# Optimization experiments

Hardware: AMD Instinct MI355X
Metric: run time of the kernel (lower is better)

## Reference

```python
import jax, jax.numpy as jnp
import numpy as np

B = 16384
SIZES = [512, 256, 256, 128]  # layer_sizes, layer 0 = clamped input
K = 16        # settling iterations
ETA = 0.1     # eta_x, scale 'none' => effective eta per layer = 0.1
CLIP = 1.0    # dx_clip


def setup_inputs() -> dict:
    key = jax.random.key(0)
    k0, k1, k2, k3 = jax.random.split(key, 4)
    x0 = jax.random.normal(k0, (B, SIZES[0]), jnp.float32)
    # W[l]: (D_{l+1}, D_l), init scale 1/sqrt(D_{l+1}) as in torch code
    W0 = jax.random.normal(k1, (SIZES[1], SIZES[0]), jnp.float32) * (1.0 / np.sqrt(SIZES[1]))
    W1 = jax.random.normal(k2, (SIZES[2], SIZES[1]), jnp.float32) * (1.0 / np.sqrt(SIZES[2]))
    W2 = jax.random.normal(k3, (SIZES[3], SIZES[2]), jnp.float32) * (1.0 / np.sqrt(SIZES[3]))
    return {"x0": x0, "W0": W0, "W1": W1, "W2": W2}


def _f(z):
    return jnp.tanh(z)


def _f_prime(z):
    t = jnp.tanh(z)
    return 1.0 - t * t


def _settle(x0, Ws):
    """Run K settling steps. Layer 0 clamped to x0; layers 1..L free."""
    L = len(Ws)
    bsz = x0.shape[0]
    xs0 = (x0,) + tuple(jnp.zeros((bsz, w.shape[0]), x0.dtype) for w in Ws)

    def step(xs, _):
        xs = list(xs)
        # top-down predictions: preact[l] = x[l+1] @ W[l], shape (B, D_l)
        preacts = [xs[l + 1] @ Ws[l] for l in range(L)]
        errs = [xs[l] - _f(preacts[l]) for l in range(L)]
        new = [xs[0]]  # layer 0 clamped
        for l in range(1, L + 1):
            # feedback: (e[l-1] * f'(preact[l-1])) @ W[l-1].T  (tied weights)
            dx = (errs[l - 1] * _f_prime(preacts[l - 1])) @ Ws[l - 1].T
            if l < L:
                dx = dx - errs[l]
            dx = jnp.clip(dx, -CLIP, CLIP)
            new.append(xs[l] + ETA * dx)
        return tuple(new), None

    final, _ = jax.lax.scan(step, xs0, None, length=K)
    return final


def reference(x0, W0, W1, W2):
    final = _settle(x0, (W0, W1, W2))
    # return settled latent (layer L) state, shape (B, 128)
    return final[-1]
```

## Files before the change

kernel.cpp:

```cpp
#include <hip/hip_runtime.h>

typedef _Float16 half8 __attribute__((ext_vector_type(8)));
typedef float floatx4 __attribute__((ext_vector_type(4)));

#define DEV_INLINE __device__ __forceinline__

constexpr int D0 = 512, D1 = 256, D2 = 256, D3 = 128;
constexpr int NROWS = 16384;
constexpr int MBLK = 32;
constexpr int NBLK = NROWS / MBLK;
constexpr int KITERS = 16;
constexpr float ETA = 0.1f;

constexpr int OFF_WF0 = 0;
constexpr int OFF_WF1 = OFF_WF0 + D1 * D0;
constexpr int OFF_WF2 = OFF_WF1 + D2 * D1;
constexpr int OFF_WB0 = OFF_WF2 + D3 * D2;
constexpr int OFF_WB1 = OFF_WB0 + D0 * D1;
constexpr int OFF_WB2 = OFF_WB1 + D1 * D2;
constexpr int PACK_ELEMS = OFF_WB2 + D2 * D3;

__global__ void repack_kernel(const float* __restrict__ W0, const float* __restrict__ W1,
                              const float* __restrict__ W2, _Float16* __restrict__ pack) {
  int p = blockIdx.x * 256 + threadIdx.x;
  if (p >= PACK_ELEMS) return;
  const float* W; int Csrc, Nd, off; bool tr;
  if (p < OFF_WF1)      { W = W0; Csrc = D0; Nd = D0; off = OFF_WF0; tr = false; }
  else if (p < OFF_WF2) { W = W1; Csrc = D1; Nd = D1; off = OFF_WF1; tr = false; }
  else if (p < OFF_WB0) { W = W2; Csrc = D2; Nd = D2; off = OFF_WF2; tr = false; }
  else if (p < OFF_WB1) { W = W0; Csrc = D0; Nd = D1; off = OFF_WB0; tr = true;  }
  else if (p < OFF_WB2) { W = W1; Csrc = D1; Nd = D1; off = OFF_WB1; tr = true;  }
  else                  { W = W2; Csrc = D2; Nd = D3; off = OFF_WB2; tr = true;  }
  int local = p - off;
  int j  = local & 7;
  int l  = (local >> 3) & 63;
  int fr = local >> 9;
  int NT = Nd >> 4;
  int nt = fr % NT, kt = fr / NT;
  int k = kt * 32 + ((l >> 4) << 3) + j;
  int n = nt * 16 + (l & 15);
  float v = tr ? W[n * Csrc + k] : W[k * Csrc + n];
  pack[p] = (_Float16)v;
}

DEV_INLINE float fast_tanh(float x) {
  float e = __expf(2.f * x);
  return 1.f - 2.f * __builtin_amdgcn_rcpf(e + 1.f);
}

DEV_INLINE void gl_lds16(const _Float16* g, char* l) {
  __builtin_amdgcn_global_load_lds(
      (const __attribute__((address_space(1))) unsigned int*)g,
      (__attribute__((address_space(3))) unsigned int*)l, 16, 0, 0);
}

template <int RT, int KSTEPS, int NTT, int STRB, int ASd>
DEV_INLINE void mm_staged(const char* __restrict__ A, const _Float16* __restrict__ Bp,
                          int nt, int lane, char* __restrict__ wslot, floatx4* acc) {
  const int arow = lane & 15;
  const int aoff = (lane >> 4) << 4;
  const _Float16* bsrc = Bp + ((size_t)nt * 64 + lane) * 8;
  gl_lds16(bsrc, wslot);
#pragma unroll
  for (int k0 = 0; k0 < KSTEPS; ++k0) {
    if (k0 + 1 < KSTEPS) {
      gl_lds16(bsrc + (size_t)(k0 + 1) * NTT * 512, wslot + ((k0 + 1) & 1) * 1024);
      asm volatile("s_waitcnt vmcnt(1)" ::: "memory");
    } else {
      asm volatile("s_waitcnt vmcnt(0)" ::: "memory");
    }
    __builtin_amdgcn_sched_barrier(0);
    const half8 b = *(const half8*)(wslot + (k0 & 1) * 1024 + lane * 16);
#pragma unroll
    for (int rt = 0; rt < RT; ++rt) {
      int row = rt * 16 + arow;
      int byte = (row * STRB + k0 * 64 + aoff) ^ ((row & 7) << 4);
      half8 a = *(const half8*)(A + byte);
      acc[rt * ASd] = __builtin_amdgcn_mfma_f32_16x16x32_f16(a, b, acc[rt * ASd], 0, 0, 0);
    }
    asm volatile("" ::: "memory");
    __builtin_amdgcn_sched_barrier(0);
  }
}

__global__ __launch_bounds__(512)
void settle_kernel(const float* __restrict__ x0,
                   const _Float16* __restrict__ pack,
                   float* __restrict__ out) {
  extern __shared__ char lds[];
  char* AX1 = lds;
  char* AG0 = lds + 16384;
  char* AQ  = lds + 24576;
  char* AG1 = lds + 40960;
  char* AR  = lds + 57344;
  char* WSL = lds + 65536;

  const int tid  = threadIdx.x;
  const int lane = tid & 63;
  const int wave = tid >> 6;
  const int row0 = blockIdx.x * MBLK;
  const int rsub = (lane >> 4) << 2;
  const int csub = lane & 15;
  char* ws = WSL + wave * 2048;

  half8 x0r[4];
#pragma unroll
  for (int q = 0; q < 4; ++q)
#pragma unroll
    for (int rt = 0; rt < 2; ++rt)
#pragma unroll
      for (int i = 0; i < 4; ++i) {
        int row = rt * 16 + rsub + i;
        int col = (q * 8 + wave) * 16 + csub;
        float v = x0[(size_t)(row0 + row) * D0 + col];
        int li = (q * 2 + rt) * 4 + i;
        x0r[li >> 3][li & 7] = (_Float16)v;
      }

  {
    floatx4 z = {0.f, 0.f, 0.f, 0.f};
    for (int i = tid; i < 1024; i += 512) ((floatx4*)AQ)[i] = z;
    for (int i = tid; i < 512; i += 512) ((floatx4*)AR)[i] = z;
  }

  const floatx4 zf = {0.f, 0.f, 0.f, 0.f};
  floatx4 x3m[2];
#pragma unroll
  for (int i = 0; i < 2; ++i) x3m[i] = zf;

  const _Float16* Wf0 = pack + OFF_WF0;
  const _Float16* Wf1 = pack + OFF_WF1;
  const _Float16* Wf2 = pack + OFF_WF2;
  const _Float16* Wb0 = pack + OFF_WB0;
  const _Float16* Wb1 = pack + OFF_WB1;
  const _Float16* Wb2 = pack + OFF_WB2;

  {
    floatx4 dx1a[4];
#pragma unroll
    for (int i = 0; i < 4; ++i) dx1a[i] = zf;
    for (int q = 0; q < 4; ++q) {
#pragma unroll
      for (int rt = 0; rt < 2; ++rt)
#pragma unroll
        for (int i = 0; i < 4; ++i) {
          int row = rt * 16 + rsub + i;
          int colq = wave * 16 + csub;
          int li = (q * 2 + rt) * 4 + i;
          int byte = (row * 256 + colq * 2) ^ ((row & 7) << 4);
          *(_Float16*)(AG0 + byte) = x0r[li >> 3][li & 7];
        }
      __syncthreads();
#pragma unroll
      for (int ct = 0; ct < 2; ++ct)
        mm_staged<2, 4, 16, 256, 2>(AG0, Wb0 + q * 32768, wave * 2 + ct, lane, ws, &dx1a[ct]);
      __syncthreads();
    }
#pragma unroll
    for (int rt = 0; rt < 2; ++rt)
#pragma unroll
      for (int ct = 0; ct < 2; ++ct) {
        int col = (wave * 2 + ct) * 16 + csub;
#pragma unroll
        for (int i = 0; i < 4; ++i) {
          int row = rt * 16 + rsub + i;
          float dx = fminf(1.f, fmaxf(-1.f, dx1a[rt * 2 + ct][i]));
          int byte = (row * 512 + col * 2) ^ ((row & 7) << 4);
          *(_Float16*)(AX1 + byte) = (_Float16)(ETA * dx);
        }
      }
    __syncthreads();
  }

  for (int it = 1; it < KITERS; ++it) {
    floatx4 dx1a[4];
    {
#pragma unroll
      for (int i = 0; i < 4; ++i) dx1a[i] = zf;
#pragma unroll
      for (int ct = 0; ct < 2; ++ct)
        mm_staged<2, 8, 16, 512, 2>(AQ, Wf1, wave * 2 + ct, lane, ws, &dx1a[ct]);
#pragma unroll
      for (int rt = 0; rt < 2; ++rt)
#pragma unroll
        for (int ct = 0; ct < 2; ++ct) {
          int col = (wave * 2 + ct) * 16 + csub;
#pragma unroll
          for (int i = 0; i < 4; ++i) {
            int row = rt * 16 + rsub + i;
            int sb = (row * 512 + col * 2) ^ ((row & 7) << 4);
            float t = fast_tanh(dx1a[rt * 2 + ct][i]);
            float x1o = (float)*(const _Float16*)(AX1 + sb);
            float e = x1o - t;
            *(_Float16*)(AG1 + sb) = (_Float16)(e * (1.f - t * t));
            dx1a[rt * 2 + ct][i] = -e;
          }
        }
    }
    for (int q = 0; q < 4; ++q) {
      {
        floatx4 acc3[2];
#pragma unroll
        for (int i = 0; i < 2; ++i) acc3[i] = zf;
        mm_staged<2, 8, 32, 512, 1>(AX1, Wf0, q * 8 + wave, lane, ws, acc3);
        int colq = wave * 16 + csub;
#pragma unroll
        for (int rt = 0; rt < 2; ++rt)
#pragma unroll
          for (int i = 0; i < 4; ++i) {
            int row = rt * 16 + rsub + i;
            int li = (q * 2 + rt) * 4 + i;
            float t = fast_tanh(acc3[rt][i]);
            float xv = (float)x0r[li >> 3][li & 7];
            float g = (xv - t) * (1.f - t * t);
            int byte = (row * 256 + colq * 2) ^ ((row & 7) << 4);
            *(_Float16*)(AG0 + byte) = (_Float16)g;
          }
      }
      __syncthreads();
#pragma unroll
      for (int ct = 0; ct < 2; ++ct)
        mm_staged<2, 4, 16, 256, 2>(AG0, Wb0 + q * 32768, wave * 2 + ct, lane, ws, &dx1a[ct]);
      __syncthreads();
    }
#pragma unroll
    for (int rt = 0; rt < 2; ++rt)
#pragma unroll
      for (int ct = 0; ct < 2; ++ct) {
        int col = (wave * 2 + ct) * 16 + csub;
#pragma unroll
        for (int i = 0; i < 4; ++i) {
          int row = rt * 16 + rsub + i;
          int sb = (row * 512 + col * 2) ^ ((row & 7) << 4);
          float dx = fminf(1.f, fmaxf(-1.f, dx1a[rt * 2 + ct][i]));
          float x1o = (float)*(const _Float16*)(AX1 + sb);
          *(_Float16*)(AX1 + sb) = (_Float16)(x1o + ETA * dx);
        }
      }
    floatx4 dx2a[4];
    half8 g2h[2];
    {
      floatx4 p2[4];
#pragma unroll
      for (int i = 0; i < 4; ++i) p2[i] = zf;
#pragma unroll
      for (int ct = 0; ct < 2; ++ct)
        mm_staged<2, 4, 16, 256, 2>(AR, Wf2, wave * 2 + ct, lane, ws, &p2[ct]);
#pragma unroll
      for (int rt = 0; rt < 2; ++rt)
#pragma unroll
        for (int ct = 0; ct < 2; ++ct) {
          int col = (wave * 2 + ct) * 16 + csub;
#pragma unroll
          for (int i = 0; i < 4; ++i) {
            int row = rt * 16 + rsub + i;
            int sb = (row * 512 + col * 2) ^ ((row & 7) << 4);
            float t = fast_tanh(p2[rt * 2 + ct][i]);
            float x2o = (float)*(const _Float16*)(AQ + sb);
            float e = x2o - t;
            int li = (rt * 2 + ct) * 4 + i;
            g2h[li >> 3][li & 7] = (_Float16)(e * (1.f - t * t));
            dx2a[rt * 2 + ct][i] = -e;
          }
        }
    }
    {
#pragma unroll
      for (int ct = 0; ct < 2; ++ct)
        mm_staged<2, 8, 16, 512, 2>(AG1, Wb1, wave * 2 + ct, lane, ws, &dx2a[ct]);
#pragma unroll
      for (int rt = 0; rt < 2; ++rt)
#pragma unroll
        for (int ct = 0; ct < 2; ++ct) {
          int col = (wave * 2 + ct) * 16 + csub;
#pragma unroll
          for (int i = 0; i < 4; ++i) {
            int row = rt * 16 + rsub + i;
            int sb = (row * 512 + col * 2) ^ ((row & 7) << 4);
            float dx = fminf(1.f, fmaxf(-1.f, dx2a[rt * 2 + ct][i]));
            float x2o = (float)*(const _Float16*)(AQ + sb);
            *(_Float16*)(AQ + sb) = (_Float16)(x2o + ETA * dx);
          }
        }
    }
    __syncthreads();
#pragma unroll
    for (int rt = 0; rt < 2; ++rt)
#pragma unroll
      for (int ct = 0; ct < 2; ++ct) {
        int col = (wave * 2 + ct) * 16 + csub;
#pragma unroll
        for (int i = 0; i < 4; ++i) {
          int row = rt * 16 + rsub + i;
          int sb = (row * 512 + col * 2) ^ ((row & 7) << 4);
          int li = (rt * 2 + ct) * 4 + i;
          *(_Float16*)(AG1 + sb) = g2h[li >> 3][li & 7];
        }
      }
    __syncthreads();
    {
      floatx4 acc6[2];
#pragma unroll
      for (int i = 0; i < 2; ++i) acc6[i] = zf;
      mm_staged<2, 8, 8, 512, 1>(AG1, Wb2, wave, lane, ws, acc6);
      __syncthreads();
      int col = wave * 16 + csub;
#pragma unroll
      for (int rt = 0; rt < 2; ++rt)
#pragma unroll
        for (int i = 0; i < 4; ++i) {
          int row = rt * 16 + rsub + i;
          float dx = fminf(1.f, fmaxf(-1.f, acc6[rt][i]));
          float nv = x3m[rt][i] + ETA * dx;
          x3m[rt][i] = nv;
          int byte = (row * 256 + col * 2) ^ ((row & 7) << 4);
          *(_Float16*)(AR + byte) = (_Float16)nv;
        }
    }
  }

  {
    int col = wave * 16 + csub;
#pragma unroll
    for (int rt = 0; rt < 2; ++rt)
#pragma unroll
      for (int i = 0; i < 4; ++i) {
        int row = rt * 16 + rsub + i;
        out[(size_t)(row0 + row) * D3 + col] = x3m[rt][i];
      }
  }
}

extern "C" void kernel_launch(void* const* d_in, const int* in_sizes, int n_in,
                              void* d_out, int out_size, void* d_ws, size_t ws_size,
                              hipStream_t stream) {
  const float* x0 = (const float*)d_in[0];
  const float* W0 = (const float*)d_in[1];
  const float* W1 = (const float*)d_in[2];
  const float* W2 = (const float*)d_in[3];
  float* out = (float*)d_out;

  _Float16* pack = (_Float16*)d_ws;
  repack_kernel<<<(PACK_ELEMS + 255) / 256, 256, 0, stream>>>(W0, W1, W2, pack);

  (void)hipFuncSetAttribute(reinterpret_cast<const void*>(settle_kernel),
                            hipFuncAttributeMaxDynamicSharedMemorySize, 81920);
  settle_kernel<<<NBLK, 512, 81920, stream>>>(x0, pack, out);
}
```

Before: 1.098 ms.

## Load weight fragments directly into registers instead of LDS double-buffering

Replaces the per-wave global_load_lds double-buffered staging of weight fragments with plain vector loads of all K-step B fragments into registers up front, followed by the MFMA loop. This removes the explicit vmcnt waits and sched barriers so the compiler can schedule loads freely. LDS use per block drops from 80KB to 64KB, which may allow more blocks per CU. In exchange it raises register pressure (up to 8 half8 B fragments held live) and exposes global/L2 latency at the start of each matmul.

```diff
diff --git a/kernel.cpp b/kernel.cpp
--- a/kernel.cpp
+++ b/kernel.cpp
@@ -48,38 +48,32 @@
   return 1.f - 2.f * __builtin_amdgcn_rcpf(e + 1.f);
 }
 
-DEV_INLINE void gl_lds16(const _Float16* g, char* l) {
-  __builtin_amdgcn_global_load_lds(
-      (const __attribute__((address_space(1))) unsigned int*)g,
-      (__attribute__((address_space(3))) unsigned int*)l, 16, 0, 0);
+DEV_INLINE const _Float16* bpt(const _Float16* Bp, int nt, int lane) {
+  return Bp + ((size_t)nt * 64 + lane) * 8;
 }
 
 template <int RT, int KSTEPS, int NTT, int STRB, int ASd>
-DEV_INLINE void mm_staged(const char* __restrict__ A, const _Float16* __restrict__ Bp,
-                          int nt, int lane, char* __restrict__ wslot, floatx4* acc) {
+DEV_INLINE void mm_reg(const char* __restrict__ A, const _Float16* __restrict__ bsrc,
+                       int lane, floatx4* acc) {
   const int arow = lane & 15;
   const int aoff = (lane >> 4) << 4;
-  const _Float16* bsrc = Bp + ((size_t)nt * 64 + lane) * 8;
-  gl_lds16(bsrc, wslot);
+  half8 bq[KSTEPS];
+#pragma unroll
+  for (int s = 0; s < KSTEPS; ++s)
+    bq[s] = *(const half8*)(bsrc + (size_t)s * NTT * 512);
 #pragma unroll
   for (int k0 = 0; k0 < KSTEPS; ++k0) {
-    if (k0 + 1 < KSTEPS) {
-      gl_lds16(bsrc + (size_t)(k0 + 1) * NTT * 512, wslot + ((k0 + 1) & 1) * 1024);
-      asm volatile("s_waitcnt vmcnt(1)" ::: "memory");
-    } else {
-      asm volatile("s_waitcnt vmcnt(0)" ::: "memory");
-    }
-    __builtin_amdgcn_sched_barrier(0);
-    const half8 b = *(const half8*)(wslot + (k0 & 1) * 1024 + lane * 16);
+    half8 a[RT];
 #pragma unroll
     for (int rt = 0; rt < RT; ++rt) {
       int row = rt * 16 + arow;
       int byte = (row * STRB + k0 * 64 + aoff) ^ ((row & 7) << 4);
-      half8 a = *(const half8*)(A + byte);
-      acc[rt * ASd] = __builtin_amdgcn_mfma_f32_16x16x32_f16(a, b, acc[rt * ASd], 0, 0, 0);
-    }
-    asm volatile("" ::: "memory");
-    __builtin_amdgcn_sched_barrier(0);
+      a[rt] = *(const half8*)(A + byte);
+    }
+#pragma unroll
+    for (int rt = 0; rt < RT; ++rt)
+      acc[rt * ASd] =
+          __builtin_amdgcn_mfma_f32_16x16x32_f16(a[rt], bq[k0], acc[rt * ASd], 0, 0, 0);
   }
 }
 
@@ -93,7 +87,6 @@
   char* AQ  = lds + 24576;
   char* AG1 = lds + 40960;
   char* AR  = lds + 57344;
-  char* WSL = lds + 65536;
 
   const int tid  = threadIdx.x;
   const int lane = tid & 63;
@@ -101,7 +94,6 @@
   const int row0 = blockIdx.x * MBLK;
   const int rsub = (lane >> 4) << 2;
   const int csub = lane & 15;
-  char* ws = WSL + wave * 2048;
 
   half8 x0r[4];
 #pragma unroll
@@ -153,7 +145,8 @@
       __syncthreads();
 #pragma unroll
       for (int ct = 0; ct < 2; ++ct)
-        mm_staged<2, 4, 16, 256, 2>(AG0, Wb0 + q * 32768, wave * 2 + ct, lane, ws, &dx1a[ct]);
+        mm_reg<2, 4, 16, 256, 2>(AG0, bpt(Wb0 + q * 32768, wave * 2 + ct, lane), lane,
+                                 &dx1a[ct]);
       __syncthreads();
     }
 #pragma unroll
@@ -179,7 +172,7 @@
       for (int i = 0; i < 4; ++i) dx1a[i] = zf;
 #pragma unroll
       for (int ct = 0; ct < 2; ++ct)
-        mm_staged<2, 8, 16, 512, 2>(AQ, Wf1, wave * 2 + ct, lane, ws, &dx1a[ct]);
+        mm_reg<2, 8, 16, 512, 2>(AQ, bpt(Wf1, wave * 2 + ct, lane), lane, &dx1a[ct]);
 #pragma unroll
       for (int rt = 0; rt < 2; ++rt)
 #pragma unroll
@@ -202,7 +195,7 @@
         floatx4 acc3[2];
 #pragma unroll
         for (int i = 0; i < 2; ++i) acc3[i] = zf;
-        mm_staged<2, 8, 32, 512, 1>(AX1, Wf0, q * 8 + wave, lane, ws, acc3);
+        mm_reg<2, 8, 32, 512, 1>(AX1, bpt(Wf0, q * 8 + wave, lane), lane, acc3);
         int colq = wave * 16 + csub;
 #pragma unroll
         for (int rt = 0; rt < 2; ++rt)
@@ -220,7 +213,8 @@
       __syncthreads();
 #pragma unroll
       for (int ct = 0; ct < 2; ++ct)
-        mm_staged<2, 4, 16, 256, 2>(AG0, Wb0 + q * 32768, wave * 2 + ct, lane, ws, &dx1a[ct]);
+        mm_reg<2, 4, 16, 256, 2>(AG0, bpt(Wb0 + q * 32768, wave * 2 + ct, lane), lane,
+                                 &dx1a[ct]);
       __syncthreads();
     }
 #pragma unroll
@@ -245,7 +239,7 @@
       for (int i = 0; i < 4; ++i) p2[i] = zf;
 #pragma unroll
       for (int ct = 0; ct < 2; ++ct)
-        mm_staged<2, 4, 16, 256, 2>(AR, Wf2, wave * 2 + ct, lane, ws, &p2[ct]);
+        mm_reg<2, 4, 16, 256, 2>(AR, bpt(Wf2, wave * 2 + ct, lane), lane, &p2[ct]);
 #pragma unroll
       for (int rt = 0; rt < 2; ++rt)
 #pragma unroll
@@ -267,7 +261,7 @@
     {
 #pragma unroll
       for (int ct = 0; ct < 2; ++ct)
-        mm_staged<2, 8, 16, 512, 2>(AG1, Wb1, wave * 2 + ct, lane, ws, &dx2a[ct]);
+        mm_reg<2, 8, 16, 512, 2>(AG1, bpt(Wb1, wave * 2 + ct, lane), lane, &dx2a[ct]);
 #pragma unroll
       for (int rt = 0; rt < 2; ++rt)
 #pragma unroll
@@ -302,7 +296,7 @@
       floatx4 acc6[2];
 #pragma unroll
       for (int i = 0; i < 2; ++i) acc6[i] = zf;
-      mm_staged<2, 8, 8, 512, 1>(AG1, Wb2, wave, lane, ws, acc6);
+      mm_reg<2, 8, 8, 512, 1>(AG1, bpt(Wb2, wave, lane), lane, acc6);
       __syncthreads();
       int col = wave * 16 + csub;
 #pragma unroll
@@ -344,6 +338,6 @@
   repack_kernel<<<(PACK_ELEMS + 255) / 256, 256, 0, stream>>>(W0, W1, W2, pack);
 
   (void)hipFuncSetAttribute(reinterpret_cast<const void*>(settle_kernel),
-                            hipFuncAttributeMaxDynamicSharedMemorySize, 81920);
-  settle_kernel<<<NBLK, 512, 81920, stream>>>(x0, pack, out);
-}
+                            hipFuncAttributeMaxDynamicSharedMemorySize, 65536);
+  settle_kernel<<<NBLK, 512, 65536, stream>>>(x0, pack, out);
+}
```

Result: slower. 1.188 ms (+8.2%).
